# Optimization experiments

Hardware: AMD Instinct MI355X
Metric: run time of the kernel (lower is better)

## Reference

```python
import jax, jax.numpy as jnp
import numpy as np

NUM_USERS = 50000
NUM_ITEMS = 50000
LATENT_DIM = 64
NUM_INTERACTIONS = 1600000
N_LAYERS = 4  # 4 ODE blocks, euler 1-step each == 4 LightGCN propagations


def setup_inputs() -> dict:
    key = jax.random.key(0)
    k1, k2, k3, k4, k5 = jax.random.split(key, 5)
    user_emb = 0.1 * jax.random.normal(k1, (NUM_USERS, LATENT_DIM), dtype=jnp.float32)
    item_emb = 0.1 * jax.random.normal(k2, (NUM_ITEMS, LATENT_DIM), dtype=jnp.float32)
    eu = jax.random.randint(k3, (NUM_INTERACTIONS,), 0, NUM_USERS, dtype=jnp.int32)
    ei = jax.random.randint(jax.random.fold_in(k3, 1), (NUM_INTERACTIONS,), 0, NUM_ITEMS, dtype=jnp.int32)
    edge_index = jnp.stack([eu, ei])  # [2, E] user->item interactions
    users = jax.random.randint(k4, (4096,), 0, NUM_USERS, dtype=jnp.int32)
    items = jax.random.randint(k5, (4096,), 0, NUM_ITEMS, dtype=jnp.int32)
    return {"user_emb": user_emb, "item_emb": item_emb,
            "edge_index": edge_index, "users": users, "items": items}


def _graph(edge_index):
    # Symmetric bipartite graph over n_users + n_items nodes, normalized D^-1/2 A D^-1/2.
    eu, ei = edge_index[0], edge_index[1] + NUM_USERS
    rows = jnp.concatenate([eu, ei])
    cols = jnp.concatenate([ei, eu])
    n = NUM_USERS + NUM_ITEMS
    deg = jax.ops.segment_sum(jnp.ones_like(rows, dtype=jnp.float32), rows, num_segments=n)
    dinv = jnp.where(deg > 0, jax.lax.rsqrt(jnp.maximum(deg, 1.0)), 0.0)
    w = dinv[rows] * dinv[cols]  # [2E]
    return rows, cols, w


def _propagate(x, rows, cols, w):
    # sparse matmul: out[r] += w_e * x[c]  (irregular gather + segment-sum)
    n = NUM_USERS + NUM_ITEMS
    return jax.ops.segment_sum(x[cols] * w[:, None], rows, num_segments=n)


def _computer(user_emb, item_emb, edge_index):
    rows, cols, w = _graph(edge_index)
    e0 = jnp.concatenate([user_emb, item_emb])  # [N, d]
    # fixed-time euler: block_k(x) = x + A x; residual subtraction leaves A x
    embs = [e0]
    x = e0
    for _ in range(N_LAYERS):
        x = _propagate(x, rows, cols, w)
        embs.append(x)
    light_out = jnp.mean(jnp.stack(embs, axis=1), axis=1)  # [N, d]
    return light_out[:NUM_USERS], light_out[NUM_USERS:]


def reference(user_emb, item_emb, edge_index, users, items):
    all_users, all_items = _computer(user_emb, item_emb, edge_index)
    u = all_users[users]
    i = all_items[items]
    gamma = jnp.sum(u * i, axis=1)  # [B]
    return gamma
```

## Files before the change

kernel.cpp:

```cpp
#include <hip/hip_runtime.h>

#define LAT 64
#define ELLC 64
#define RB 128
#define RBSH 7
#define MAXBUK 1024
#define RPT 8

#define SC0 64.0f
#define RSC 3.0f

typedef float f32x2 __attribute__((ext_vector_type(2)));

__global__ void __launch_bounds__(1024)
bin_k(const int* __restrict__ eu, const int* __restrict__ ei,
      int* __restrict__ gcur, unsigned int* __restrict__ bbuf,
      int2* __restrict__ ovf, int* __restrict__ ovfc,
      int E, int U, int nbuk, int cap, int ovf_cap) {
    __shared__ int lcnt[MAXBUK];
    __shared__ int lbase[MAXBUK];
    for (int i = threadIdx.x; i < nbuk; i += blockDim.x) lcnt[i] = 0;
    __syncthreads();
    int tid = blockIdx.x * blockDim.x + threadIdx.x;
    int stride = gridDim.x * blockDim.x;
    int ru[RPT], rc[RPT];
    int ne = 0;
#pragma unroll
    for (int k = 0; k < RPT; ++k) {
        int d = tid + k * stride;
        if (d < E) {
            int u = eu[d], c = ei[d] + U;
            ru[k] = u; rc[k] = c; ne = k + 1;
            atomicAdd(&lcnt[u >> RBSH], 1);
            atomicAdd(&lcnt[c >> RBSH], 1);
        }
    }
    __syncthreads();
    for (int b = threadIdx.x; b < nbuk; b += blockDim.x)
        lbase[b] = atomicAdd(&gcur[b], lcnt[b]);
    __syncthreads();
#pragma unroll
    for (int k = 0; k < RPT; ++k) {
        if (k < ne) {
            int u = ru[k], c = rc[k];
            int b = u >> RBSH;
            int pos = atomicAdd(&lbase[b], 1);
            if (pos < cap)
                bbuf[(size_t)b * cap + pos] = ((unsigned)(u & (RB - 1)) << 17) | (unsigned)c;
            else { int o = atomicAdd(ovfc, 1); if (o < ovf_cap) ovf[o] = make_int2(u, c); }
            b = c >> RBSH;
            pos = atomicAdd(&lbase[b], 1);
            if (pos < cap)
                bbuf[(size_t)b * cap + pos] = ((unsigned)(c & (RB - 1)) << 17) | (unsigned)u;
            else { int o = atomicAdd(ovfc, 1); if (o < ovf_cap) ovf[o] = make_int2(c, u); }
        }
    }
}

__global__ void __launch_bounds__(1024)
build_k(const unsigned int* __restrict__ bbuf, const int* __restrict__ gcur,
        int* __restrict__ cnt, int* __restrict__ colE, float* __restrict__ dinv,
        const float* __restrict__ ue, const float* __restrict__ ie,
        unsigned char* __restrict__ y0,
        int2* __restrict__ rovf, int* __restrict__ rovfc,
        int N, int U, int cap, int rovf_cap) {
    __shared__ int lcnt[RB];
    __shared__ float ldv[RB];
    __shared__ int ell[RB * ELLC];
    int b = blockIdx.x;
    for (int i = threadIdx.x; i < RB; i += blockDim.x) lcnt[i] = 0;
    for (int i = threadIdx.x; i < RB * ELLC; i += blockDim.x) ell[i] = 0;
    __syncthreads();
    int nb = min(gcur[b], cap);
    const unsigned int* src = bbuf + (size_t)b * cap;
    for (int e = threadIdx.x; e < nb; e += blockDim.x) {
        unsigned w = src[e];
        int r7 = (int)(w >> 17);
        int c = (int)(w & 0x1FFFF);
        int pos = atomicAdd(&lcnt[r7], 1);
        if (pos < ELLC) ell[(r7 << 6) + pos] = c;
        else {
            int o = atomicAdd(rovfc, 1);
            if (o < rovf_cap) rovf[o] = make_int2((b << RBSH) + r7, c);
        }
    }
    __syncthreads();
    for (int i = threadIdx.x; i < RB; i += blockDim.x) {
        int r = (b << RBSH) + i;
        if (r < N) {
            int d = lcnt[i];
            cnt[r] = d;
            float dv = (d > 0) ? rsqrtf((float)d) : 0.0f;
            dinv[r] = dv;
            ldv[i] = dv;
        }
    }
    __syncthreads();
    int r0 = b << RBSH;
    int rows = min(RB, N - r0);
    for (int w = threadIdx.x; w < rows * 16; w += blockDim.x) {
        int i = w >> 4, j = w & 15;
        int r = r0 + i;
        const float* s = (r < U) ? (ue + (size_t)r * LAT) : (ie + (size_t)(r - U) * LAT);
        float4 f = ((const float4*)s)[j];
        float sc = SC0 * ldv[i];
        int p = __builtin_amdgcn_cvt_pk_fp8_f32(sc * f.x, sc * f.y, 0, false);
        p = __builtin_amdgcn_cvt_pk_fp8_f32(sc * f.z, sc * f.w, p, true);
        ((unsigned*)y0)[(size_t)r * 16 + j] = (unsigned)p;
    }
    uint4* dst = (uint4*)(colE + (size_t)r0 * ELLC);
    const uint4* lsrc = (const uint4*)ell;
    for (int w = threadIdx.x; w < rows * 16; w += blockDim.x)
        dst[w] = lsrc[w];
}

__global__ void __launch_bounds__(1024)
fix_k(const int2* __restrict__ ovf, const int* __restrict__ ovfc,
      int* __restrict__ cnt, int* __restrict__ colE, float* __restrict__ dinv,
      const float* __restrict__ ue, const float* __restrict__ ie,
      unsigned char* __restrict__ y0,
      int2* __restrict__ rovf, int* __restrict__ rovfc,
      int ovf_cap, int rovf_cap, int U) {
    int n = min(*ovfc, ovf_cap);
    for (int i = threadIdx.x; i < n; i += blockDim.x) {
        int r = ovf[i].x, c = ovf[i].y;
        int pos = atomicAdd(&cnt[r], 1);
        if (pos < ELLC) colE[(size_t)r * ELLC + pos] = c;
        else { int o = atomicAdd(rovfc, 1); if (o < rovf_cap) rovf[o] = make_int2(r, c); }
    }
    __syncthreads();
    for (int i = threadIdx.x; i < n; i += blockDim.x) {
        int r = ovf[i].x;
        int d = cnt[r];
        dinv[r] = (d > 0) ? rsqrtf((float)d) : 0.0f;
    }
    __syncthreads();
    for (int w = threadIdx.x; w < n * 16; w += blockDim.x) {
        int o = w >> 4, j = w & 15;
        int r = ovf[o].x;
        const float* s = (r < U) ? (ue + (size_t)r * LAT) : (ie + (size_t)(r - U) * LAT);
        float4 f = ((const float4*)s)[j];
        float sc = SC0 * dinv[r];
        int p = __builtin_amdgcn_cvt_pk_fp8_f32(sc * f.x, sc * f.y, 0, false);
        p = __builtin_amdgcn_cvt_pk_fp8_f32(sc * f.z, sc * f.w, p, true);
        ((unsigned*)y0)[(size_t)r * 16 + j] = (unsigned)p;
    }
}

__device__ __forceinline__ void acc_word(unsigned w, f32x2* a) {
    a[0] += __builtin_amdgcn_cvt_pk_f32_fp8((int)w, false);
    a[1] += __builtin_amdgcn_cvt_pk_f32_fp8((int)w, true);
}

__global__ void __launch_bounds__(256, 8)
prop_h_k(const int* __restrict__ cnt, const int* __restrict__ colE,
         const float* __restrict__ dinv, const unsigned char* __restrict__ yin,
         unsigned char* __restrict__ yout,
         const int* __restrict__ users, const int* __restrict__ items,
         float* __restrict__ qacc,
         const float* __restrict__ ue, const float* __restrict__ ie,
         const int2* __restrict__ rovf, const int* __restrict__ rovfc,
         int rovf_cap, int B, int U, int first, int N, float inv_sin) {
    int wave = blockIdx.x * (blockDim.x >> 6) + (threadIdx.x >> 6);
    int lane = threadIdx.x & 63;
    int NW = (N + 3) >> 2;
    if (wave >= NW) {
        int qw = wave - NW;
        if (qw >= 2 * B) return;
        int node = (qw < B) ? users[qw] : (items[qw - B] + U);
        if (first) {
            float v = (node < U) ? ue[(size_t)node * LAT + lane]
                                 : ie[(size_t)(node - U) * LAT + lane];
            qacc[qw * LAT + lane] = v;
        } else {
            float di = dinv[node];
            unsigned bb = yin[(size_t)node * LAT + lane];
            f32x2 yv = __builtin_amdgcn_cvt_pk_f32_fp8((int)bb, false);
            qacc[qw * LAT + lane] += (di > 0.0f) ? yv[0] * inv_sin / di : 0.0f;
        }
        return;
    }
    int grp  = lane >> 4;
    int gbase = lane & 48;
    int q  = (lane >> 2) & 3;
    int s4 = lane & 3;
    int node = (wave << 2) + grp;
    int nadr = min(node, N - 1);
    int len = (node < N) ? min(cnt[nadr], ELLC) : 0;
    const int* cp = colE + (size_t)nadr * ELLC;
    int wmax = len;
    wmax = max(wmax, __shfl_xor(wmax, 16));
    wmax = max(wmax, __shfl_xor(wmax, 32));
    wmax = __builtin_amdgcn_readfirstlane(wmax);
    int gl = lane & 15;
    int ca0 = cp[gl];
    int ca1 = (wmax > 16) ? cp[16 + gl] : 0;
    int ca2 = (wmax > 32) ? cp[32 + gl] : 0;
    int ca3 = (wmax > 48) ? cp[48 + gl] : 0;
    const uint4* y16 = (const uint4*)yin;

    f32x2 acc[8];
#pragma unroll
    for (int j = 0; j < 8; ++j) acc[j] = (f32x2)(0.f);

#pragma unroll
    for (int c = 0; c < 4; ++c) {
        int cac = (c == 0) ? ca0 : (c == 1) ? ca1 : (c == 2) ? ca2 : ca3;
#pragma unroll
        for (int si = 0; si < 4; ++si) {
            int s = (c << 2) + si;
            if ((s << 2) < wmax) {
                int col = __shfl(cac, gbase + (si << 2) + q);
                if ((s << 2) + q < len) {
                    uint4 v = y16[(size_t)col * 4 + s4];
                    acc_word(v.x, acc + 0); acc_word(v.y, acc + 2);
                    acc_word(v.z, acc + 4); acc_word(v.w, acc + 6);
                }
            }
        }
    }
    int novf = min(*rovfc, rovf_cap);
    for (int o = 0; o < novf; ++o) {
        int2 eo = rovf[o];
        if (eo.x == node && q == 0) {
            uint4 vv = y16[(size_t)eo.y * 4 + s4];
            acc_word(vv.x, acc + 0); acc_word(vv.y, acc + 2);
            acc_word(vv.z, acc + 4); acc_word(vv.w, acc + 6);
        }
    }
    {
        bool hi = (lane & 4) != 0;
        f32x2 s[4], k[4];
#pragma unroll
        for (int i = 0; i < 4; ++i) { k[i] = hi ? acc[4 + i] : acc[i]; s[i] = hi ? acc[i] : acc[4 + i]; }
#pragma unroll
        for (int i = 0; i < 4; ++i) {
            f32x2 t;
            t.x = __shfl_xor(s[i].x, 4);
            t.y = __shfl_xor(s[i].y, 4);
            acc[i] = k[i] + t;
        }
    }
    {
        bool hi = (lane & 8) != 0;
        f32x2 s[2], k[2];
#pragma unroll
        for (int i = 0; i < 2; ++i) { k[i] = hi ? acc[2 + i] : acc[i]; s[i] = hi ? acc[i] : acc[2 + i]; }
#pragma unroll
        for (int i = 0; i < 2; ++i) {
            f32x2 t;
            t.x = __shfl_xor(s[i].x, 8);
            t.y = __shfl_xor(s[i].y, 8);
            acc[i] = k[i] + t;
        }
    }
    float dv = dinv[nadr];
    float f = dv * dv * RSC;
    int pk = __builtin_amdgcn_cvt_pk_fp8_f32(f * acc[0].x, f * acc[0].y, 0, false);
    pk = __builtin_amdgcn_cvt_pk_fp8_f32(f * acc[1].x, f * acc[1].y, pk, true);
    if (node < N) {
        int b2 = (lane >> 2) & 1, b3 = (lane >> 3) & 1;
        ((unsigned*)yout)[(size_t)node * 16 + (s4 << 2) + (b2 << 1) + b3] = (unsigned)pk;
    }
}

__global__ void __launch_bounds__(256, 8)
last_k(const int* __restrict__ cnt, const int* __restrict__ colE,
       const float* __restrict__ dinv, const unsigned char* __restrict__ y3,
       const int* __restrict__ users, const int* __restrict__ items,
       float* __restrict__ qacc,
       const int2* __restrict__ rovf, const int* __restrict__ rovfc,
       int rovf_cap, int B, int U, int N, float inv_s3) {
    int wave = blockIdx.x * (blockDim.x >> 6) + (threadIdx.x >> 6);
    int lane = threadIdx.x & 63;
    int grp  = lane >> 4;
    int gbase = lane & 48;
    int q  = (lane >> 2) & 3;
    int s4 = lane & 3;
    int e = (wave << 2) + grp;
    int ecl = min(e, 2 * B - 1);
    int node = (ecl < B) ? users[ecl] : (items[ecl - B] + U);
    bool valid = (e < 2 * B);
    int len = valid ? min(cnt[node], ELLC) : 0;
    const int* cp = colE + (size_t)node * ELLC;
    int wmax = len;
    wmax = max(wmax, __shfl_xor(wmax, 16));
    wmax = max(wmax, __shfl_xor(wmax, 32));
    wmax = __builtin_amdgcn_readfirstlane(wmax);
    int gl = lane & 15;
    int ca0 = cp[gl];
    int ca1 = (wmax > 16) ? cp[16 + gl] : 0;
    int ca2 = (wmax > 32) ? cp[32 + gl] : 0;
    int ca3 = (wmax > 48) ? cp[48 + gl] : 0;
    const uint4* y16 = (const uint4*)y3;

    f32x2 acc[8];
#pragma unroll
    for (int j = 0; j < 8; ++j) acc[j] = (f32x2)(0.f);

#pragma unroll
    for (int c = 0; c < 4; ++c) {
        int cac = (c == 0) ? ca0 : (c == 1) ? ca1 : (c == 2) ? ca2 : ca3;
#pragma unroll
        for (int si = 0; si < 4; ++si) {
            int s = (c << 2) + si;
            if ((s << 2) < wmax) {
                int col = __shfl(cac, gbase + (si << 2) + q);
                if ((s << 2) + q < len) {
                    uint4 v = y16[(size_t)col * 4 + s4];
                    acc_word(v.x, acc + 0); acc_word(v.y, acc + 2);
                    acc_word(v.z, acc + 4); acc_word(v.w, acc + 6);
                }
            }
        }
    }
    int novf = min(*rovfc, rovf_cap);
    for (int o = 0; o < novf; ++o) {
        int2 eo = rovf[o];
        if (valid && eo.x == node && q == 0) {
            uint4 vv = y16[(size_t)eo.y * 4 + s4];
            acc_word(vv.x, acc + 0); acc_word(vv.y, acc + 2);
            acc_word(vv.z, acc + 4); acc_word(vv.w, acc + 6);
        }
    }
    {
        bool hi = (lane & 4) != 0;
        f32x2 s[4], k[4];
#pragma unroll
        for (int i = 0; i < 4; ++i) { k[i] = hi ? acc[4 + i] : acc[i]; s[i] = hi ? acc[i] : acc[4 + i]; }
#pragma unroll
        for (int i = 0; i < 4; ++i) {
            f32x2 t;
            t.x = __shfl_xor(s[i].x, 4);
            t.y = __shfl_xor(s[i].y, 4);
            acc[i] = k[i] + t;
        }
    }
    {
        bool hi = (lane & 8) != 0;
        f32x2 s[2], k[2];
#pragma unroll
        for (int i = 0; i < 2; ++i) { k[i] = hi ? acc[2 + i] : acc[i]; s[i] = hi ? acc[i] : acc[2 + i]; }
#pragma unroll
        for (int i = 0; i < 2; ++i) {
            f32x2 t;
            t.x = __shfl_xor(s[i].x, 8);
            t.y = __shfl_xor(s[i].y, 8);
            acc[i] = k[i] + t;
        }
    }
    int b2 = (lane >> 2) & 1, b3 = (lane >> 3) & 1;
    int widx = (s4 << 2) + (b2 << 1) + b3;
    float dv = dinv[node];
    float x4s = dv * inv_s3;
    float r3 = (dv > 0.f) ? inv_s3 / dv : 0.f;
    unsigned w3 = ((const unsigned*)y3)[(size_t)node * 16 + widx];
    f32x2 lo3 = __builtin_amdgcn_cvt_pk_f32_fp8((int)w3, false);
    f32x2 hi3 = __builtin_amdgcn_cvt_pk_f32_fp8((int)w3, true);
    if (valid) {
        float4* qp = (float4*)(qacc + (size_t)e * LAT + (widx << 2));
        float4 old = *qp;
        old.x += x4s * acc[0].x + r3 * lo3[0];
        old.y += x4s * acc[0].y + r3 * lo3[1];
        old.z += x4s * acc[1].x + r3 * hi3[0];
        old.w += x4s * acc[1].y + r3 * hi3[1];
        *qp = old;
    }
}

__global__ void dot_k(const float* __restrict__ qacc, float* __restrict__ out, int B) {
    int wave = blockIdx.x * (blockDim.x >> 6) + (threadIdx.x >> 6);
    int lane = threadIdx.x & 63;
    if (wave >= B) return;
    float au = qacc[(size_t)wave * LAT + lane];
    float ai = qacc[(size_t)(wave + B) * LAT + lane];
    float p = au * ai;
#pragma unroll
    for (int off = 32; off > 0; off >>= 1) p += __shfl_down(p, off);
    if (lane == 0) out[wave] = p * (1.0f / 25.0f);
}

extern "C" void kernel_launch(void* const* d_in, const int* in_sizes, int n_in,
                              void* d_out, int out_size, void* d_ws, size_t ws_size,
                              hipStream_t stream) {
    const float* ue = (const float*)d_in[0];
    const float* ie = (const float*)d_in[1];
    const int* edge = (const int*)d_in[2];
    const int* users = (const int*)d_in[3];
    const int* items = (const int*)d_in[4];

    const int U = in_sizes[0] / LAT;
    const int I = in_sizes[1] / LAT;
    const int N = U + I;
    const int E = in_sizes[2] / 2;
    const int B = in_sizes[3];
    const int* eu = edge;
    const int* ei = edge + E;

    const int nbuk = (N + RB - 1) / RB;
    const int cap = ((2 * E / nbuk) * 5 / 4 + 255) & ~255;

    char* ws = (char*)d_ws;
    size_t off = 0;
    auto alloc = [&](size_t bytes) -> void* {
        void* p = ws + off;
        off += (bytes + 255) & ~(size_t)255;
        return p;
    };
    int*           cnt  = (int*)alloc((size_t)4 * N);
    float*         dinv = (float*)alloc((size_t)4 * N);
    int*           colE = (int*)alloc((size_t)4 * N * ELLC);
    unsigned char* yA   = (unsigned char*)alloc((size_t)N * LAT);
    unsigned char* yB   = (unsigned char*)alloc((size_t)N * LAT);
    float*         qacc = (float*)alloc((size_t)4 * 2 * B * LAT);
    unsigned*      bbuf = (unsigned*)alloc((size_t)4 * nbuk * cap);
    size_t zoff = off;
    int*      gcur = (int*)alloc((size_t)4 * nbuk);
    int*      ovfc = (int*)alloc(256);
    size_t zbytes = off - zoff;
    size_t remain = (ws_size > off + 256) ? (ws_size - off - 256) : 0;
    int ovf_cap = (int)min((size_t)131072, remain / (2 * sizeof(int2)));
    int2* ovf  = (int2*)alloc((size_t)ovf_cap * sizeof(int2));
    int2* rovf = (int2*)alloc((size_t)ovf_cap * sizeof(int2));
    int* rovfc = ovfc + 16;

    hipError_t _e = hipMemsetAsync(gcur, 0, zbytes, stream); (void)_e;

    const int tb = 256;

    bin_k<<<256, 1024, 0, stream>>>(eu, ei, gcur, bbuf, ovf, ovfc, E, U, nbuk, cap, ovf_cap);
    build_k<<<nbuk, 1024, 0, stream>>>(bbuf, gcur, cnt, colE, dinv, ue, ie, yA,
                                       rovf, rovfc, N, U, cap, ovf_cap);
    fix_k<<<1, 1024, 0, stream>>>(ovf, ovfc, cnt, colE, dinv, ue, ie, yA,
                                  rovf, rovfc, ovf_cap, ovf_cap, U);

    const int wpb = tb / 64;
    const int NW = (N + 3) >> 2;
    int pgrid = (NW + 2 * B + wpb - 1) / wpb;

    unsigned char* yin = yA;
    unsigned char* yout = yB;
    float s_in = SC0;
    for (int layer = 0; layer < 3; ++layer) {
        prop_h_k<<<pgrid, tb, 0, stream>>>(cnt, colE, dinv, yin, yout,
                                           users, items, qacc, ue, ie, rovf, rovfc,
                                           ovf_cap, B, U, layer == 0 ? 1 : 0, N,
                                           1.0f / s_in);
        s_in *= RSC;
        unsigned char* tmp = yin; yin = yout; yout = tmp;
    }

    int lwaves = (2 * B + 3) >> 2;
    last_k<<<(lwaves + wpb - 1) / wpb, tb, 0, stream>>>(cnt, colE, dinv, yin,
                                                        users, items, qacc,
                                                        rovf, rovfc, ovf_cap,
                                                        B, U, N, 1.0f / s_in);

    dot_k<<<(B + wpb - 1) / wpb, tb, 0, stream>>>(qacc, (float*)d_out, B);
}
```

Measured before the change: 218.3 us.

## Coalesce edge binning writes via shared-memory staging with coarser 256-row buckets

The binning kernel now uses 256-row buckets (400 bins) and stages bucket entries in shared memory, flushing them to global memory as aligned 16-word vector stores in phases instead of issuing scattered 4-byte stores. The build kernel runs two blocks per coarse bucket, and each block filters entries by the sub-bucket bit encoded in the packed word. This targets the uncoalesced scatter writes in the binning pass. In exchange, each build block now reads twice as many entries, and the bin kernel adds many block-wide syncs plus about 55KB of shared memory per block.

Result: slower. 223.3 us (+2.3%).

```diff
diff --git a/kernel.cpp b/kernel.cpp
--- a/kernel.cpp
+++ b/kernel.cpp
@@ -4,7 +4,9 @@
 #define ELLC 64
 #define RB 128
 #define RBSH 7
-#define MAXBUK 1024
+#define NBIN 400
+#define RBSHB 8
+#define STAGE 32
 #define RPT 8
 
 #define SC0 64.0f
@@ -17,8 +19,11 @@
       int* __restrict__ gcur, unsigned int* __restrict__ bbuf,
       int2* __restrict__ ovf, int* __restrict__ ovfc,
       int E, int U, int nbuk, int cap, int ovf_cap) {
-    __shared__ int lcnt[MAXBUK];
-    __shared__ int lbase[MAXBUK];
+    __shared__ int lcnt[NBIN];
+    __shared__ int gflush[NBIN];
+    __shared__ int rbase[NBIN];
+    __shared__ int okf[NBIN];
+    __shared__ unsigned stage[NBIN * STAGE];
     for (int i = threadIdx.x; i < nbuk; i += blockDim.x) lcnt[i] = 0;
     __syncthreads();
     int tid = blockIdx.x * blockDim.x + threadIdx.x;
@@ -31,29 +36,60 @@
         if (d < E) {
             int u = eu[d], c = ei[d] + U;
             ru[k] = u; rc[k] = c; ne = k + 1;
-            atomicAdd(&lcnt[u >> RBSH], 1);
-            atomicAdd(&lcnt[c >> RBSH], 1);
-        }
-    }
-    __syncthreads();
-    for (int b = threadIdx.x; b < nbuk; b += blockDim.x)
-        lbase[b] = atomicAdd(&gcur[b], lcnt[b]);
-    __syncthreads();
-#pragma unroll
-    for (int k = 0; k < RPT; ++k) {
-        if (k < ne) {
-            int u = ru[k], c = rc[k];
-            int b = u >> RBSH;
-            int pos = atomicAdd(&lbase[b], 1);
-            if (pos < cap)
-                bbuf[(size_t)b * cap + pos] = ((unsigned)(u & (RB - 1)) << 17) | (unsigned)c;
-            else { int o = atomicAdd(ovfc, 1); if (o < ovf_cap) ovf[o] = make_int2(u, c); }
-            b = c >> RBSH;
-            pos = atomicAdd(&lbase[b], 1);
-            if (pos < cap)
-                bbuf[(size_t)b * cap + pos] = ((unsigned)(c & (RB - 1)) << 17) | (unsigned)u;
-            else { int o = atomicAdd(ovfc, 1); if (o < ovf_cap) ovf[o] = make_int2(c, u); }
-        }
+            atomicAdd(&lcnt[u >> RBSHB], 1);
+            atomicAdd(&lcnt[c >> RBSHB], 1);
+        }
+    }
+    __syncthreads();
+    for (int b = threadIdx.x; b < nbuk; b += blockDim.x) {
+        int cb = lcnt[b];
+        int rb = atomicAdd(&gcur[b], cb);
+        rbase[b] = rb;
+        okf[b] = (rb + cb <= cap);
+        gflush[b] = (rb + 15) & ~15;
+        lcnt[b] = 0;
+    }
+    __syncthreads();
+    int gq = threadIdx.x >> 2, j = threadIdx.x & 3;
+    for (int h = 0; h < 2 * RPT; ++h) {
+        int k = h >> 1;
+        if (k < ne && ((threadIdx.x >> 9) & 1) == (h & 1)) {
+#pragma unroll
+            for (int t = 0; t < 2; ++t) {
+                int r = t ? rc[k] : ru[k];
+                int c = t ? ru[k] : rc[k];
+                int b = r >> RBSHB;
+                unsigned w = ((unsigned)(r & 255) << 17) | (unsigned)c;
+                int pos = atomicAdd(&lcnt[b], 1);
+                if (okf[b]) {
+                    int rb = rbase[b];
+                    int gpos = rb + pos;
+                    if (gpos < ((rb + 15) & ~15))
+                        bbuf[(size_t)b * cap + gpos] = w;
+                    else
+                        stage[(b << 5) + (gpos & (STAGE - 1))] = w;
+                } else { int o = atomicAdd(ovfc, 1); if (o < ovf_cap) ovf[o] = make_int2(r, c); }
+            }
+        }
+        __syncthreads();
+        for (int b = gq; b < nbuk; b += 256) {
+            if (!okf[b]) continue;
+            int end = rbase[b] + lcnt[b];
+            int f = gflush[b];
+            while (f + 16 <= end) {
+                uint4 v = *(const uint4*)&stage[(b << 5) + (f & (STAGE - 1)) + (j << 2)];
+                *(uint4*)&bbuf[(size_t)b * cap + f + (j << 2)] = v;
+                f += 16;
+            }
+            if (j == 0) gflush[b] = f;
+        }
+        __syncthreads();
+    }
+    for (int b = gq; b < nbuk; b += 256) {
+        if (!okf[b]) continue;
+        int end = rbase[b] + lcnt[b];
+        for (int g = gflush[b] + j; g < end; g += 4)
+            bbuf[(size_t)b * cap + g] = stage[(b << 5) + (g & (STAGE - 1))];
     }
 }
 
@@ -68,20 +104,23 @@
     __shared__ float ldv[RB];
     __shared__ int ell[RB * ELLC];
     int b = blockIdx.x;
+    int bb = b >> 1, sub = b & 1;
     for (int i = threadIdx.x; i < RB; i += blockDim.x) lcnt[i] = 0;
     for (int i = threadIdx.x; i < RB * ELLC; i += blockDim.x) ell[i] = 0;
     __syncthreads();
-    int nb = min(gcur[b], cap);
-    const unsigned int* src = bbuf + (size_t)b * cap;
+    int nb = min(gcur[bb], cap);
+    const unsigned int* src = bbuf + (size_t)bb * cap;
     for (int e = threadIdx.x; e < nb; e += blockDim.x) {
         unsigned w = src[e];
-        int r7 = (int)(w >> 17);
-        int c = (int)(w & 0x1FFFF);
-        int pos = atomicAdd(&lcnt[r7], 1);
-        if (pos < ELLC) ell[(r7 << 6) + pos] = c;
-        else {
-            int o = atomicAdd(rovfc, 1);
-            if (o < rovf_cap) rovf[o] = make_int2((b << RBSH) + r7, c);
+        if ((int)((w >> 24) & 1) == sub) {
+            int r7 = (int)(w >> 17) & 127;
+            int c = (int)(w & 0x1FFFF);
+            int pos = atomicAdd(&lcnt[r7], 1);
+            if (pos < ELLC) ell[(r7 << 6) + pos] = c;
+            else {
+                int o = atomicAdd(rovfc, 1);
+                if (o < rovf_cap) rovf[o] = make_int2((b << RBSH) + r7, c);
+            }
         }
     }
     __syncthreads();
@@ -397,7 +436,8 @@
     const int* eu = edge;
     const int* ei = edge + E;
 
-    const int nbuk = (N + RB - 1) / RB;
+    const int nbuk = (N + 255) >> 8;
+    const int nbld = (N + RB - 1) / RB;
     const int cap = ((2 * E / nbuk) * 5 / 4 + 255) & ~255;
 
     char* ws = (char*)d_ws;
@@ -429,7 +469,7 @@
     const int tb = 256;
 
     bin_k<<<256, 1024, 0, stream>>>(eu, ei, gcur, bbuf, ovf, ovfc, E, U, nbuk, cap, ovf_cap);
-    build_k<<<nbuk, 1024, 0, stream>>>(bbuf, gcur, cnt, colE, dinv, ue, ie, yA,
+    build_k<<<nbld, 1024, 0, stream>>>(bbuf, gcur, cnt, colE, dinv, ue, ie, yA,
                                        rovf, rovfc, N, U, cap, ovf_cap);
     fix_k<<<1, 1024, 0, stream>>>(ovf, ovfc, cnt, colE, dinv, ue, ie, yA,
                                   rovf, rovfc, ovf_cap, ovf_cap, U);
```
